# Kernel optimization log

Hardware: AMD Instinct MI355X
Metric: run time of the kernel (lower is better)

Reference implementation:

```python
import jax, jax.numpy as jnp
import numpy as np

EPS = 1e-5


def _knn_group(q, p, kk):
    """q: [3,Nq] query points, p: [3,M] reference points. Returns
    features [4,Nq,kk] = (residual xyz, distance) and neighbors [3,Nq,kk]."""
    qt, pt = q.T, p.T  # [Nq,3], [M,3]
    d2 = (jnp.sum(qt * qt, axis=1)[:, None]
          + jnp.sum(pt * pt, axis=1)[None, :]
          - 2.0 * qt @ pt.T)                       # [Nq,M] squared dists
    _, idx = jax.lax.top_k(-d2, kk)                 # kk nearest -> [Nq,kk]
    nn = pt[idx]                                    # [Nq,kk,3]
    resi = nn - qt[:, None, :]
    dist = jnp.linalg.norm(resi, axis=-1, keepdims=True)
    feat = jnp.concatenate([resi, dist], axis=-1)   # [Nq,kk,4]
    return feat.transpose(2, 0, 1), nn.transpose(2, 0, 1)


def _group_norm(x, groups, w, b):
    B, C, N, K = x.shape
    xg = x.reshape(B, groups, C // groups, N, K)
    mu = xg.mean(axis=(2, 3, 4), keepdims=True)
    var = xg.var(axis=(2, 3, 4), keepdims=True)
    xg = (xg - mu) * jax.lax.rsqrt(var + EPS)
    return xg.reshape(B, C, N, K) * w[None, :, None, None] + b[None, :, None, None]


def _forward(points0, points1, w1, b1, gn1_w, gn1_b, w2, b2, gn2_w, gn2_b,
             k, wt_np, perm_np):
    B, _, N = points0.shape
    feats, grouped = [], []
    for i in range(B):  # per-sample loop: split sizes are data-dependent (as in original)
        N0 = int(N * wt_np[i, 0]); N1 = N - N0
        k0 = int(k * wt_np[i, 0]); k1 = k - k0
        newp = jnp.concatenate([points0[i][:, perm_np[i, 0, :N0]],
                                points1[i][:, perm_np[i, 1, :N1]]], axis=-1)  # [3,N]
        f0, g0 = _knn_group(newp, points0[i], k0)
        f1, g1 = _knn_group(newp, points1[i], k1)
        feats.append(jnp.concatenate([f0, f1], axis=-1))
        grouped.append(jnp.concatenate([g0, g1], axis=-1))
    x = jnp.stack(feats)        # [B,4,N,k]
    gp = jnp.stack(grouped)     # [B,3,N,k]
    # 1x1 conv -> GroupNorm -> ReLU, twice
    x = jnp.einsum('bcnk,oc->bonk', x, w1) + b1[None, :, None, None]
    x = jax.nn.relu(_group_norm(x, w1.shape[0] // 8, gn1_w, gn1_b))
    x = jnp.einsum('bcnk,oc->bonk', x, w2) + b2[None, :, None, None]
    x = jax.nn.relu(_group_norm(x, w2.shape[0] // 8, gn2_w, gn2_b))
    scores = jnp.max(x, axis=1)                 # [B,N,k]
    wts = jax.nn.softmax(scores, axis=-1)       # softmax over neighbors
    return jnp.sum(wts[:, None, :, :] * gp, axis=-1)  # [B,3,N]


def setup_inputs() -> dict:
    key = jax.random.key(0)
    B, N, K = 8, 4096, 32
    C1, C2 = 32, 64
    ks = jax.random.split(key, 8)
    points0 = jax.random.normal(ks[0], (B, 3, N), jnp.float32)
    points1 = jax.random.normal(ks[1], (B, 3, N), jnp.float32)
    weighted_t = jax.random.uniform(ks[2], (B, 2), jnp.float32, 0.25, 0.75)
    perm = jax.vmap(lambda kk: jax.random.permutation(kk, N))(
        jax.random.split(ks[3], B * 2)).reshape(B, 2, N).astype(jnp.int32)
    w1 = 0.1 * jax.random.normal(ks[4], (C1, 4), jnp.float32)
    b1 = jnp.zeros((C1,), jnp.float32)
    gn1_w = jnp.ones((C1,), jnp.float32)
    gn1_b = jnp.zeros((C1,), jnp.float32)
    w2 = 0.1 * jax.random.normal(ks[5], (C2, C1), jnp.float32)
    b2 = jnp.zeros((C2,), jnp.float32)
    gn2_w = jnp.ones((C2,), jnp.float32)
    gn2_b = jnp.zeros((C2,), jnp.float32)
    return dict(points0=points0, points1=points1, k=K, weighted_t=weighted_t,
                perm=perm, w1=w1, b1=b1, gn1_w=gn1_w, gn1_b=gn1_b,
                w2=w2, b2=b2, gn2_w=gn2_w, gn2_b=gn2_b)


def reference(points0, points1, k, weighted_t, perm, w1, b1, gn1_w, gn1_b,
              w2, b2, gn2_w, gn2_b):
    wt_np = np.asarray(weighted_t)   # concrete: drives static split sizes
    perm_np = np.asarray(perm)
    return _forward(points0, points1, w1, b1, gn1_w, gn1_b, w2, b2,
                    gn2_w, gn2_b, int(k), wt_np, perm_np)
```

## Files before the change

### kernel.cpp

```cpp
#include <hip/hip_runtime.h>
#include <math.h>

#define RQ 6
constexpr int WRANKS = 768;
constexpr int WCH = 12;

typedef __attribute__((ext_vector_type(8))) short s8v;
typedef __attribute__((ext_vector_type(4))) float f32x4;

__device__ inline unsigned short f2bf(float x) {
    const unsigned int u = __float_as_uint(x);
    return (unsigned short)((u + 0x7FFFu + ((u >> 16) & 1u)) >> 16);
}

__constant__ float ZB[63] = {
    -2.1539f, -1.8627f, -1.6759f, -1.5341f, -1.4178f, -1.3180f, -1.2299f, -1.1503f,
    -1.0775f, -1.0100f, -0.9468f, -0.8871f, -0.8305f, -0.7764f, -0.7245f, -0.6745f,
    -0.6261f, -0.5791f, -0.5334f, -0.4888f, -0.4451f, -0.4023f, -0.3601f, -0.3186f,
    -0.2776f, -0.2372f, -0.1971f, -0.1573f, -0.1178f, -0.0784f, -0.0392f,  0.0000f,
     0.0392f,  0.0784f,  0.1178f,  0.1573f,  0.1971f,  0.2372f,  0.2776f,  0.3186f,
     0.3601f,  0.4023f,  0.4451f,  0.4888f,  0.5334f,  0.5791f,  0.6261f,  0.6745f,
     0.7245f,  0.7764f,  0.8305f,  0.8871f,  0.9468f,  1.0100f,  1.0775f,  1.1503f,
     1.2299f,  1.3180f,  1.4178f,  1.5341f,  1.6759f,  1.8627f,  2.1539f };

__global__ __launch_bounds__(1024) void zbin_kernel(
    const float* __restrict__ p0, const float* __restrict__ p1,
    float4* __restrict__ sp, int* __restrict__ starts, int N)
{
    __shared__ int cnt[64], off[64], cur[64];
    const int t = threadIdx.x;
    const int bl = blockIdx.x;
    const int b = bl >> 1, list = bl & 1;
    const float* rb = (list ? p1 : p0) + (size_t)(b * 3) * N;
    if (t < 64) { cnt[t] = 0; cur[t] = 0; }
    __syncthreads();
    int mybin[4]; float mx[4], my[4], mz[4];
    for (int i = 0; i < 4; ++i) {
        const int idx = i * 1024 + t;
        const float z = rb[2 * N + idx];
        mx[i] = rb[idx]; my[i] = rb[N + idx]; mz[i] = z;
        int bin = 0;
#pragma unroll
        for (int s = 32; s; s >>= 1)
            if (bin + s <= 63 && z >= ZB[bin + s - 1]) bin += s;
        mybin[i] = bin;
        atomicAdd(&cnt[bin], 1);
    }
    __syncthreads();
    if (t < 64) {
        const int v = cnt[t];
        int x = v;
#pragma unroll
        for (int o = 1; o < 64; o <<= 1) {
            const int y = __shfl_up(x, o);
            if (t >= o) x += y;
        }
        off[t] = x - v;
        starts[bl * 65 + t] = x - v;
        if (t == 63) starts[bl * 65 + 64] = x;
    }
    __syncthreads();
    for (int i = 0; i < 4; ++i) {
        const int bin = mybin[i];
        const int pos = off[bin] + atomicAdd(&cur[bin], 1);
        sp[(size_t)bl * 4096 + pos] =
            make_float4(mx[i], my[i], mz[i],
                        fmaf(mx[i], mx[i], fmaf(my[i], my[i], mz[i] * mz[i])));
    }
}


__device__ __forceinline__ void cpush(unsigned key, unsigned pos, unsigned Tu,
                                      bool valid,
                                      unsigned* __restrict__ ck,
                                      unsigned* __restrict__ cp,
                                      int& cnt)
{
    const bool pred = valid && (key <= Tu);
    const unsigned long long bal = __ballot(pred);
    const unsigned below = __builtin_amdgcn_mbcnt_hi(
        (unsigned)(bal >> 32), __builtin_amdgcn_mbcnt_lo((unsigned)bal, 0u));
    const unsigned idx = (unsigned)cnt + below;
    if (pred && idx < 64u) { ck[idx] = key; cp[idx] = pos; }
    cnt += (int)__popcll(bal);
}

__device__ __forceinline__ void cscan(const float4* __restrict__ L,
                                      int bs, int be,
                                      float qx, float qy, float qz, float qq,
                                      unsigned Tu,
                                      unsigned* __restrict__ ck,
                                      unsigned* __restrict__ cp,
                                      int& cnt, int lane)
{
    for (int p = bs; p < be; p += 64) {
        const int pos = p + lane;
        const float4 pc = L[min(pos, be - 1)];
        const float dt = fmaf(qz, pc.z, fmaf(qy, pc.y, qx * pc.x));
        const float d = fmaxf(fmaf(-2.f, dt, pc.w + qq), 0.f);
        cpush(__float_as_uint(d), (unsigned)pos, Tu, pos < be, ck, cp, cnt);
    }
}

__device__ __forceinline__ void sort2_write(
    const unsigned* __restrict__ ck0, const unsigned* __restrict__ cp0, int cnt0,
    const float4* __restrict__ L0, int kk0, int ob0,
    const unsigned* __restrict__ ck1, const unsigned* __restrict__ cp1, int cnt1,
    const float4* __restrict__ L1, int kk1, int ob1,
    float qx, float qy, float qz, float4* __restrict__ feat, int lane)
{
    unsigned vk0 = (lane < cnt0) ? ck0[lane] : 0xFFFFFFFFu;
    unsigned vp0 = (lane < cnt0) ? cp0[lane] : 0xFFFFFFFFu;
    unsigned vk1 = (lane < cnt1) ? ck1[lane] : 0xFFFFFFFFu;
    unsigned vp1 = (lane < cnt1) ? cp1[lane] : 0xFFFFFFFFu;
#pragma unroll
    for (int k2 = 2; k2 <= 64; k2 <<= 1) {
#pragma unroll
        for (int jj = k2 >> 1; jj; jj >>= 1) {
            const unsigned yk0 = __shfl_xor(vk0, jj), yp0 = __shfl_xor(vp0, jj);
            const unsigned yk1 = __shfl_xor(vk1, jj), yp1 = __shfl_xor(vp1, jj);
            const bool keepmin = (((lane & jj) == 0) == ((lane & k2) == 0));
            const bool lt0 = (vk0 < yk0) || ((vk0 == yk0) && (vp0 < yp0));
            const bool s0 = keepmin ? (!lt0) : lt0;
            vk0 = s0 ? yk0 : vk0; vp0 = s0 ? yp0 : vp0;
            const bool lt1 = (vk1 < yk1) || ((vk1 == yk1) && (vp1 < yp1));
            const bool s1 = keepmin ? (!lt1) : lt1;
            vk1 = s1 ? yk1 : vk1; vp1 = s1 ? yp1 : vp1;
        }
    }
    if (lane < kk0) {
        const float4 pc = L0[vp0 & 4095u];
        const float rx = pc.x - qx, ry = pc.y - qy, rz = pc.z - qz;
        feat[ob0 + lane] =
            make_float4(rx, ry, rz, sqrtf(fmaf(rx, rx, fmaf(ry, ry, rz * rz))));
    }
    if (lane < kk1) {
        const float4 pc = L1[vp1 & 4095u];
        const float rx = pc.x - qx, ry = pc.y - qy, rz = pc.z - qz;
        feat[ob1 + lane] =
            make_float4(rx, ry, rz, sqrtf(fmaf(rx, rx, fmaf(ry, ry, rz * rz))));
    }
}

__device__ __forceinline__ void sort_write(
    const unsigned* __restrict__ ck, const unsigned* __restrict__ cp, int cnt,
    const float4* __restrict__ L, int kk, int obase,
    float qx, float qy, float qz, float4* __restrict__ feat, int lane)
{
    unsigned vk = (lane < cnt) ? ck[lane] : 0xFFFFFFFFu;
    unsigned vp = (lane < cnt) ? cp[lane] : 0xFFFFFFFFu;
#pragma unroll
    for (int k2 = 2; k2 <= 64; k2 <<= 1) {
#pragma unroll
        for (int jj = k2 >> 1; jj; jj >>= 1) {
            const unsigned yk = __shfl_xor(vk, jj);
            const unsigned yp = __shfl_xor(vp, jj);
            const bool keepmin = (((lane & jj) == 0) == ((lane & k2) == 0));
            const bool lt = (vk < yk) || ((vk == yk) && (vp < yp));
            const bool sely = keepmin ? (!lt) : lt;
            vk = sely ? yk : vk;
            vp = sely ? yp : vp;
        }
    }
    if (lane < kk) {
        const float4 pc = L[vp & 4095u];
        const float rx = pc.x - qx, ry = pc.y - qy, rz = pc.z - qz;
        feat[obase + lane] =
            make_float4(rx, ry, rz, sqrtf(fmaf(rx, rx, fmaf(ry, ry, rz * rz))));
    }
}

__device__ __forceinline__ void qpush(unsigned (&kh)[RQ], unsigned (&kl)[RQ],
                                      unsigned key, unsigned pos)
{
    bool cb[RQ];
#pragma unroll
    for (int s = 0; s < RQ; ++s) cb[s] = key < kh[s];
#pragma unroll
    for (int s = RQ - 1; s >= 1; --s) {
        kh[s] = cb[s - 1] ? kh[s - 1] : (cb[s] ? key : kh[s]);
        kl[s] = cb[s - 1] ? kl[s - 1] : (cb[s] ? pos : kl[s]);
    }
    kh[0] = cb[0] ? key : kh[0];
    kl[0] = cb[0] ? pos : kl[0];
}

__device__ __forceinline__ void pop_extract(
    unsigned (&kh)[RQ], unsigned (&kl)[RQ], int kk,
    const float4* __restrict__ L, int obase,
    float qx, float qy, float qz, float4* __restrict__ feat, int lane)
{
    unsigned mwin = 0;
    for (int rr = 0; rr < kk; ++rr) {
        unsigned gg = kh[0];
#pragma unroll
        for (int off = 32; off; off >>= 1) gg = min(gg, __shfl_xor(gg, off));
        const bool tied = (kh[0] == gg);
        unsigned mc;
        const unsigned long long bal = __ballot(tied);
        if (bal & (bal - 1)) {
            mc = tied ? kl[0] : 0xFFFFFFFFu;
#pragma unroll
            for (int off = 32; off; off >>= 1) mc = min(mc, __shfl_xor(mc, off));
        } else {
            mc = __shfl(kl[0], (int)__ffsll((long long)bal) - 1);
        }
        const bool w = tied && (kl[0] == mc);
        if (lane == rr) mwin = mc;
#pragma unroll
        for (int s = 0; s < RQ - 1; ++s) {
            kh[s] = w ? kh[s + 1] : kh[s];
            kl[s] = w ? kl[s + 1] : kl[s];
        }
        kh[RQ - 1] = w ? 0xFFFFFFFFu : kh[RQ - 1];
        kl[RQ - 1] = w ? 0xFFFFFFFFu : kl[RQ - 1];
    }
    if (lane < kk) {
        const float4 pc = L[mwin & 4095u];
        const float rx = pc.x - qx, ry = pc.y - qy, rz = pc.z - qz;
        feat[obase + lane] =
            make_float4(rx, ry, rz, sqrtf(fmaf(rx, rx, fmaf(ry, ry, rz * rz))));
    }
}

__device__ __forceinline__ void fallback_full(
    const float4* __restrict__ L, int Npts, int kk, int obase,
    float qx, float qy, float qz, float qq,
    float4* __restrict__ feat, int lane)
{
    unsigned kh[RQ], kl[RQ];
#pragma unroll
    for (int s = 0; s < RQ; ++s) { kh[s] = 0xFFFFFFFFu; kl[s] = 0xFFFFFFFFu; }
    for (int p = 0; p < Npts; p += 64) {
        const int pos = p + lane;
        const float4 pc = L[min(pos, Npts - 1)];
        const float dt = fmaf(qz, pc.z, fmaf(qy, pc.y, qx * pc.x));
        const float d = fmaxf(fmaf(-2.f, dt, pc.w + qq), 0.f);
        const unsigned key = (pos < Npts) ? __float_as_uint(d) : 0xFFFFFFFFu;
        qpush(kh, kl, key, (unsigned)pos);
    }
    pop_extract(kh, kl, kk, L, obase, qx, qy, qz, feat, lane);
}

__global__ __launch_bounds__(256, 4) void knn_kernel(
    const float* __restrict__ p0, const float* __restrict__ p1,
    const float* __restrict__ wt, const int* __restrict__ perm,
    const float4* __restrict__ sp, const int* __restrict__ starts,
    float4* __restrict__ feat, float4* __restrict__ newp, int N)
{
    __shared__ unsigned ck0s[256], cp0s[256], ck1s[256], cp1s[256];
    const int lane = threadIdx.x & 63;
    const int wv = threadIdx.x >> 6;
    const int gwave = (int)((blockIdx.x * 256 + threadIdx.x) >> 6);
    const int b = gwave / N;
    const int n = gwave - b * N;
    const int q = b * N + n;

    unsigned* __restrict__ ck0 = ck0s + wv * 64;
    unsigned* __restrict__ cp0 = cp0s + wv * 64;
    unsigned* __restrict__ ck1 = ck1s + wv * 64;
    unsigned* __restrict__ cp1 = cp1s + wv * 64;

    const float wt0 = wt[b * 2];
    const int N0 = (int)(N * wt0);
    const int k0 = (int)(32 * wt0);
    const int kk0 = k0, kk1 = 32 - k0;

    int j; const float* src;
    if (n < N0) { j = perm[(b * 2) * N + n];            src = p0; }
    else        { j = perm[(b * 2 + 1) * N + (n - N0)]; src = p1; }
    const float qx = __uint_as_float(__builtin_amdgcn_readfirstlane(
                         __float_as_uint(src[(b * 3) * N + j])));
    const float qy = __uint_as_float(__builtin_amdgcn_readfirstlane(
                         __float_as_uint(src[(b * 3 + 1) * N + j])));
    const float qz = __uint_as_float(__builtin_amdgcn_readfirstlane(
                         __float_as_uint(src[(b * 3 + 2) * N + j])));
    const float qq = qx * qx + qy * qy + qz * qz;

    const int bl0 = b * 2, bl1 = b * 2 + 1;
    const int stv0 = starts[bl0 * 65 + lane];
    const int stv1 = starts[bl1 * 65 + lane];

    const float bv = (lane < 63) ? ZB[lane] : 3.0e38f;
    const int qbin = __popcll(__ballot(qz >= bv));

    if (lane == 0) newp[q] = make_float4(qx, qy, qz, 0.f);

    const float4* L0 = sp + (size_t)bl0 * 4096;
    const float4* L1 = sp + (size_t)bl1 * 4096;

    const int st0 = __shfl(stv0, qbin);
    const int en0 = (qbin >= 63) ? N : __shfl(stv0, qbin + 1);
    const int st1 = __shfl(stv1, qbin);
    const int en1 = (qbin >= 63) ? N : __shfl(stv1, qbin + 1);
    int s0 = ((st0 + en0) >> 1) - WRANKS / 2;
    s0 = s0 < 0 ? 0 : (s0 > N - WRANKS ? N - WRANKS : s0);
    int s1 = ((st1 + en1) >> 1) - WRANKS / 2;
    s1 = s1 < 0 ? 0 : (s1 > N - WRANKS ? N - WRANKS : s1);
    const int e0 = s0 + WRANKS, e1 = s1 + WRANKS;

    const float4* Lb0 = L0 + s0 + lane;
    const float4* Lb1 = L1 + s1 + lane;
    unsigned k0v[WCH], k1v[WCH];
    unsigned mn0 = 0xFFFFFFFFu, mn1 = 0xFFFFFFFFu;
    {
        float4 A0[3], A1[3], B0[3], B1[3];
#pragma unroll
        for (int c = 0; c < 3; ++c) { A0[c] = Lb0[c << 6]; A1[c] = Lb1[c << 6]; }
#pragma unroll
        for (int g = 0; g < 4; ++g) {
            if (g < 3) {
#pragma unroll
                for (int c = 0; c < 3; ++c) {
                    B0[c] = Lb0[(g * 3 + 3 + c) << 6];
                    B1[c] = Lb1[(g * 3 + 3 + c) << 6];
                }
            }
#pragma unroll
            for (int c = 0; c < 3; ++c) {
                const int ch = g * 3 + c;
                {
                    const float dt = fmaf(qz, A0[c].z, fmaf(qy, A0[c].y, qx * A0[c].x));
                    k0v[ch] = __float_as_uint(fmaxf(fmaf(-2.f, dt, A0[c].w + qq), 0.f));
                    mn0 = min(mn0, k0v[ch]);
                }
                {
                    const float dt = fmaf(qz, A1[c].z, fmaf(qy, A1[c].y, qx * A1[c].x));
                    k1v[ch] = __float_as_uint(fmaxf(fmaf(-2.f, dt, A1[c].w + qq), 0.f));
                    mn1 = min(mn1, k1v[ch]);
                }
            }
            if (g < 3) {
#pragma unroll
                for (int c = 0; c < 3; ++c) { A0[c] = B0[c]; A1[c] = B1[c]; }
            }
        }
    }

    unsigned x0 = mn0, x1 = mn1;
#pragma unroll
    for (int k2 = 2; k2 <= 64; k2 <<= 1) {
#pragma unroll
        for (int jj = k2 >> 1; jj; jj >>= 1) {
            const unsigned y0 = __shfl_xor(x0, jj);
            const unsigned y1 = __shfl_xor(x1, jj);
            const bool keepmin = (((lane & jj) == 0) == ((lane & k2) == 0));
            x0 = keepmin ? min(x0, y0) : (x0 > y0 ? x0 : y0);
            x1 = keepmin ? min(x1, y1) : (x1 > y1 ? x1 : y1);
        }
    }
    const unsigned Tu0 = (unsigned)__shfl((int)x0, kk0 - 1);
    const unsigned Tu1 = (unsigned)__shfl((int)x1, kk1 - 1);
    const float T0f = __uint_as_float(Tu0);
    const float T1f = __uint_as_float(Tu1);

    int cnt0 = 0, cnt1 = 0;
#pragma unroll
    for (int ch = 0; ch < WCH; ++ch) {
        cpush(k0v[ch], (unsigned)(s0 + (ch << 6) + lane), Tu0, true, ck0, cp0, cnt0);
        cpush(k1v[ch], (unsigned)(s1 + (ch << 6) + lane), Tu1, true, ck1, cp1, cnt1);
    }

    {
        const int binL = __popcll(__ballot(stv0 <= s0)) - 1;
        if (s0 > 0) {
            const int bs = __shfl(stv0, binL);
            if (bs < s0) cscan(L0, bs, s0, qx, qy, qz, qq, Tu0, ck0, cp0, cnt0, lane);
            for (int jb = binL - 1; jb >= 0; --jb) {
                const float dz = qz - ZB[jb];
                if (dz * dz * 0.99999f > T0f) break;
                const int bs2 = __shfl(stv0, jb);
                const int be2 = __shfl(stv0, jb + 1);
                cscan(L0, bs2, be2, qx, qy, qz, qq, Tu0, ck0, cp0, cnt0, lane);
            }
        }
        if (e0 < N) {
            const int binR = __popcll(__ballot(stv0 <= e0)) - 1;
            const int re = (binR >= 63) ? N : __shfl(stv0, binR + 1);
            if (e0 < re) cscan(L0, e0, re, qx, qy, qz, qq, Tu0, ck0, cp0, cnt0, lane);
            for (int jb = binR + 1; jb <= 63; ++jb) {
                const float dz = ZB[jb - 1] - qz;
                if (dz * dz * 0.99999f > T0f) break;
                const int bs2 = __shfl(stv0, jb);
                const int be2 = (jb >= 63) ? N : __shfl(stv0, jb + 1);
                cscan(L0, bs2, be2, qx, qy, qz, qq, Tu0, ck0, cp0, cnt0, lane);
            }
        }
        const int binL1 = __popcll(__ballot(stv1 <= s1)) - 1;
        if (s1 > 0) {
            const int bs = __shfl(stv1, binL1);
            if (bs < s1) cscan(L1, bs, s1, qx, qy, qz, qq, Tu1, ck1, cp1, cnt1, lane);
            for (int jb = binL1 - 1; jb >= 0; --jb) {
                const float dz = qz - ZB[jb];
                if (dz * dz * 0.99999f > T1f) break;
                const int bs2 = __shfl(stv1, jb);
                const int be2 = __shfl(stv1, jb + 1);
                cscan(L1, bs2, be2, qx, qy, qz, qq, Tu1, ck1, cp1, cnt1, lane);
            }
        }
        if (e1 < N) {
            const int binR1 = __popcll(__ballot(stv1 <= e1)) - 1;
            const int re = (binR1 >= 63) ? N : __shfl(stv1, binR1 + 1);
            if (e1 < re) cscan(L1, e1, re, qx, qy, qz, qq, Tu1, ck1, cp1, cnt1, lane);
            for (int jb = binR1 + 1; jb <= 63; ++jb) {
                const float dz = ZB[jb - 1] - qz;
                if (dz * dz * 0.99999f > T1f) break;
                const int bs2 = __shfl(stv1, jb);
                const int be2 = (jb >= 63) ? N : __shfl(stv1, jb + 1);
                cscan(L1, bs2, be2, qx, qy, qz, qq, Tu1, ck1, cp1, cnt1, lane);
            }
        }
    }

    const int ob0 = (q << 5), ob1 = (q << 5) + k0;
    if ((cnt0 <= 64) && (cnt1 <= 64)) {
        sort2_write(ck0, cp0, cnt0, L0, kk0, ob0,
                    ck1, cp1, cnt1, L1, kk1, ob1,
                    qx, qy, qz, feat, lane);
    } else {
        if (cnt0 <= 64) sort_write(ck0, cp0, cnt0, L0, kk0, ob0, qx, qy, qz, feat, lane);
        else            fallback_full(L0, N, kk0, ob0, qx, qy, qz, qq, feat, lane);
        if (cnt1 <= 64) sort_write(ck1, cp1, cnt1, L1, kk1, ob1, qx, qy, qz, feat, lane);
        else            fallback_full(L1, N, kk1, ob1, qx, qy, qz, qq, feat, lane);
    }
}

__global__ __launch_bounds__(256) void moment_stats_kernel(
    const float4* __restrict__ feat, float* __restrict__ stats1, int N)
{
    const int t = threadIdx.x, lane = t & 63;
    const int bpb = 64;
    const int b = blockIdx.x / bpb;
    const int ppb = (N * 32) / bpb;
    const size_t base = (size_t)b * N * 32 + (size_t)(blockIdx.x % bpb) * ppb;
    float a[14];
#pragma unroll
    for (int i = 0; i < 14; ++i) a[i] = 0.f;
    for (int i = t; i < ppb; i += 256) {
        const float4 f = feat[base + i];
        a[0] += f.x; a[1] += f.y; a[2] += f.z; a[3] += f.w;
        a[4] = fmaf(f.x, f.x, a[4]);  a[5] = fmaf(f.x, f.y, a[5]);
        a[6] = fmaf(f.x, f.z, a[6]);  a[7] = fmaf(f.x, f.w, a[7]);
        a[8] = fmaf(f.y, f.y, a[8]);  a[9] = fmaf(f.y, f.z, a[9]);
        a[10] = fmaf(f.y, f.w, a[10]); a[11] = fmaf(f.z, f.z, a[11]);
        a[12] = fmaf(f.z, f.w, a[12]); a[13] = fmaf(f.w, f.w, a[13]);
    }
#pragma unroll
    for (int i = 0; i < 14; ++i) {
        float x = a[i];
#pragma unroll
        for (int o = 32; o; o >>= 1) x += __shfl_down(x, o);
        a[i] = x;
    }
    __shared__ float sm[14];
    if (t < 14) sm[t] = 0.f;
    __syncthreads();
    if (lane == 0) {
#pragma unroll
        for (int i = 0; i < 14; ++i) atomicAdd(&sm[i], a[i]);
    }
    __syncthreads();
    if (t < 14) atomicAdd(&stats1[b * 14 + t], sm[t]);
}

template <int MODE>
__global__ __launch_bounds__(256) void conv2_pass_kernel(
    const float4* __restrict__ feat,
    const float* __restrict__ w1, const float* __restrict__ b1,
    const float* __restrict__ gn1w, const float* __restrict__ gn1b,
    const float* __restrict__ stats1,
    const float* __restrict__ w2, const float* __restrict__ b2,
    const float* __restrict__ gn2w, const float* __restrict__ gn2b,
    float* __restrict__ stats2,
    const float4* __restrict__ newp, float* __restrict__ out,
    int N, float inv_cnt)
{
    const int t = threadIdx.x, lane = t & 63, wv = t >> 6;
    const int quad = lane >> 4, col = lane & 15;
    const int bpb = (N * 32) / 512;
    const int b = blockIdx.x / bpb;
    const int pblock = (blockIdx.x - b * bpb) * 512;
    const size_t pbase = (size_t)b * N * 32 + pblock + wv * 128;

    __shared__ float sfin[24];
    __shared__ float sacc[16];
    __shared__ unsigned short h_lds[512 * 40];
    __shared__ float ssc[512];

    if (t < 16) sacc[t] = 0.f;
    if (t < 4) {
        const float cnt = (float)(N * 32);
        const float* mm = stats1 + b * 14;
        const float S0 = mm[0], S1 = mm[1], S2 = mm[2], S3 = mm[3];
        float sum = 0.f, sq = 0.f;
        for (int cch = 0; cch < 8; ++cch) {
            const int cid = t * 8 + cch;
            const float4 w = ((const float4*)w1)[cid];
            const float bb = b1[cid];
            const float ws = w.x * S0 + w.y * S1 + w.z * S2 + w.w * S3;
            const float wMw =
                w.x * w.x * mm[4] + w.y * w.y * mm[8] + w.z * w.z * mm[11] +
                w.w * w.w * mm[13] +
                2.f * (w.x * w.y * mm[5] + w.x * w.z * mm[6] + w.x * w.w * mm[7] +
                       w.y * w.z * mm[9] + w.y * w.w * mm[10] + w.z * w.w * mm[12]);
            sum += cnt * bb + ws;
            sq += cnt * bb * bb + 2.f * bb * ws + wMw;
        }
        const float mu = sum * inv_cnt, var = sq * inv_cnt - mu * mu;
        sfin[2 * t] = mu; sfin[2 * t + 1] = rsqrtf(var + 1e-5f);
    }
    if (MODE == 1 && t >= 4 && t < 12) {
        const int g = t - 4;
        const float S = stats2[b * 16 + g], Q = stats2[b * 16 + 8 + g];
        const float mu = S * inv_cnt, var = Q * inv_cnt - mu * mu;
        sfin[8 + 2 * g] = mu; sfin[8 + 2 * g + 1] = rsqrtf(var + 1e-5f);
    }
    __syncthreads();

    const int c1 = lane & 31, pt = lane >> 5;
    const float4 w1r = ((const float4*)w1)[c1];
    const float b1c = b1[c1];
    const int g1 = c1 >> 3;
    const float sc1 = sfin[2 * g1 + 1] * gn1w[c1];
    const float sh1 = gn1b[c1] - sfin[2 * g1] * sc1;

    for (int it = 0; it < 64; ++it) {
        const size_t p = pbase + it * 2;
        const float4 f = feat[p + pt];
        const float y = b1c + w1r.x * f.x + w1r.y * f.y + w1r.z * f.z + w1r.w * f.w;
        const float h = fmaxf(0.f, fmaf(y, sc1, sh1));
        h_lds[(wv * 128 + it * 2 + pt) * 40 + c1] = f2bf(h);
    }

    s8v afr[4];
#pragma unroll
    for (int T = 0; T < 4; ++T) {
        const int row = T * 16 + col;
#pragma unroll
        for (int j2 = 0; j2 < 8; ++j2)
            afr[T][j2] = (short)f2bf(w2[row * 32 + quad * 8 + j2]);
    }

    float b2v[4][4], sc2v[4][4], sh2v[4][4];
#pragma unroll
    for (int T = 0; T < 4; ++T)
#pragma unroll
        for (int r4 = 0; r4 < 4; ++r4) {
            const int cch = T * 16 + quad * 4 + r4;
            b2v[T][r4] = b2[cch];
            if (MODE == 1) {
                const int g2 = cch >> 3;
                const float sc = sfin[8 + 2 * g2 + 1] * gn2w[cch];
                sc2v[T][r4] = sc;
                sh2v[T][r4] = gn2b[cch] - sfin[8 + 2 * g2] * sc + b2[cch] * sc;
            }
        }

    float gsum[4] = {0, 0, 0, 0}, gsq[4] = {0, 0, 0, 0};

    for (int pt16 = 0; pt16 < 8; ++pt16) {
        const int row = wv * 128 + pt16 * 16 + col;
        const s8v bfr = *(const s8v*)&h_lds[row * 40 + quad * 8];
        f32x4 acc[4];
#pragma unroll
        for (int T = 0; T < 4; ++T) {
            acc[T] = (f32x4){0.f, 0.f, 0.f, 0.f};
            acc[T] = __builtin_amdgcn_mfma_f32_16x16x32_bf16(afr[T], bfr, acc[T], 0, 0, 0);
        }
        if (MODE == 0) {
#pragma unroll
            for (int T = 0; T < 4; ++T)
#pragma unroll
                for (int r4 = 0; r4 < 4; ++r4) {
                    const float v = acc[T][r4] + b2v[T][r4];
                    gsum[T] += v;
                    gsq[T] = fmaf(v, v, gsq[T]);
                }
        } else {
            float s = -3.0e38f;
#pragma unroll
            for (int T = 0; T < 4; ++T)
#pragma unroll
                for (int r4 = 0; r4 < 4; ++r4)
                    s = fmaxf(s, fmaxf(0.f, fmaf(acc[T][r4], sc2v[T][r4], sh2v[T][r4])));
            s = fmaxf(s, __shfl_xor(s, 16));
            s = fmaxf(s, __shfl_xor(s, 32));
            if (quad == 0) ssc[wv * 128 + pt16 * 16 + col] = s;
        }
    }

    if (MODE == 0) {
#pragma unroll
        for (int T = 0; T < 4; ++T) {
#pragma unroll
            for (int o = 1; o < 16; o <<= 1) {
                gsum[T] += __shfl_xor(gsum[T], o);
                gsq[T] += __shfl_xor(gsq[T], o);
            }
            gsum[T] += __shfl_xor(gsum[T], 16);
            gsq[T] += __shfl_xor(gsq[T], 16);
        }
        if (lane == 0) {
#pragma unroll
            for (int T = 0; T < 4; ++T) {
                atomicAdd(&sacc[2 * T], gsum[T]);
                atomicAdd(&sacc[8 + 2 * T], gsq[T]);
            }
        }
        if (lane == 32) {
#pragma unroll
            for (int T = 0; T < 4; ++T) {
                atomicAdd(&sacc[2 * T + 1], gsum[T]);
                atomicAdd(&sacc[8 + 2 * T + 1], gsq[T]);
            }
        }
        __syncthreads();
        if (t < 16) atomicAdd(&stats2[b * 16 + t], sacc[t]);
    } else {
        __syncthreads();
        const int qi = t >> 4, sub = t & 15;
        const int qg = (b * N * 32 + pblock) / 32 + qi;
        const int n = qg - b * N;
        const float s0 = ssc[qi * 32 + sub], s1 = ssc[qi * 32 + 16 + sub];
        float mx = fmaxf(s0, s1);
#pragma unroll
        for (int o = 8; o; o >>= 1) mx = fmaxf(mx, __shfl_xor(mx, o));
        const float e0 = __expf(s0 - mx), e1 = __expf(s1 - mx);
        float ssum = e0 + e1;
#pragma unroll
        for (int o = 8; o; o >>= 1) ssum += __shfl_xor(ssum, o);
        const float4 qc = newp[qg];
        const float4 f0 = feat[(size_t)qg * 32 + sub];
        const float4 f1 = feat[(size_t)qg * 32 + 16 + sub];
        float ax = e0 * (qc.x + f0.x) + e1 * (qc.x + f1.x);
        float ay = e0 * (qc.y + f0.y) + e1 * (qc.y + f1.y);
        float az = e0 * (qc.z + f0.z) + e1 * (qc.z + f1.z);
#pragma unroll
        for (int o = 8; o; o >>= 1) {
            ax += __shfl_xor(ax, o);
            ay += __shfl_xor(ay, o);
            az += __shfl_xor(az, o);
        }
        if (sub == 0) {
            const float inv = 1.f / ssum;
            out[(b * 3 + 0) * N + n] = ax * inv;
            out[(b * 3 + 1) * N + n] = ay * inv;
            out[(b * 3 + 2) * N + n] = az * inv;
        }
    }
}

extern "C" void kernel_launch(void* const* d_in, const int* in_sizes, int n_in,
                              void* d_out, int out_size, void* d_ws, size_t ws_size,
                              hipStream_t stream)
{
    const float* p0   = (const float*)d_in[0];
    const float* p1   = (const float*)d_in[1];
    const float* wt   = (const float*)d_in[3];
    const int*   perm = (const int*)d_in[4];
    const float* w1   = (const float*)d_in[5];
    const float* b1   = (const float*)d_in[6];
    const float* gn1w = (const float*)d_in[7];
    const float* gn1b = (const float*)d_in[8];
    const float* w2   = (const float*)d_in[9];
    const float* b2   = (const float*)d_in[10];
    const float* gn2w = (const float*)d_in[11];
    const float* gn2b = (const float*)d_in[12];
    float* out = (float*)d_out;

    const int B = in_sizes[3] / 2;
    const int N = in_sizes[0] / (3 * B);

    char* ws = (char*)d_ws;
    float4* spts = (float4*)ws;
    size_t off = (size_t)B * 2 * 4096 * sizeof(float4);
    float4* feat = (float4*)(ws + off);       off += (size_t)B * N * 32 * sizeof(float4);
    float4* newp = (float4*)(ws + off);       off += (size_t)B * N * sizeof(float4);
    float* stats1 = (float*)(ws + off);       off += (size_t)B * 14 * sizeof(float);
    float* stats2 = (float*)(ws + off);       off += (size_t)B * 16 * sizeof(float);
    int* starts = (int*)(ws + off);

    hipMemsetAsync(stats1, 0, (size_t)B * 30 * sizeof(float), stream);

    const float inv_cnt = 1.f / (8.f * (float)N * 32.f);

    zbin_kernel<<<B * 2, 1024, 0, stream>>>(p0, p1, spts, starts, N);

    knn_kernel<<<(B * N) / 4, 256, 0, stream>>>(
        p0, p1, wt, perm, spts, starts, feat, newp, N);

    moment_stats_kernel<<<B * 64, 256, 0, stream>>>(feat, stats1, N);

    conv2_pass_kernel<0><<<(B * N * 32) / 512, 256, 0, stream>>>(
        feat, w1, b1, gn1w, gn1b, stats1, w2, b2, gn2w, gn2b, stats2,
        newp, out, N, inv_cnt);

    conv2_pass_kernel<1><<<(B * N * 32) / 512, 256, 0, stream>>>(
        feat, w1, b1, gn1w, gn1b, stats1, w2, b2, gn2w, gn2b, stats2,
        newp, out, N, inv_cnt);
}
```

Baseline: 343.0 us.

## Split query gather into its own kernel, shrink KNN window, pack candidate LDS

Moves the permuted query-point gather out of the KNN kernel into a separate gather_kernel that writes newp, so each KNN wave reads one float4 instead of doing a dependent perm lookup and three scattered loads. It also shrinks the initial candidate window from 768 to 512 ranks (12 to 8 chunks), replaces the software-pipelined window load with a straight batch of loads, and packs key/position candidates into uint2 in LDS. The smaller window reduces register pressure and first-pass work, but gives a looser threshold, which can lead to more neighbor-bin scans or fallbacks. It also adds one extra kernel launch.

```diff
diff --git a/kernel.cpp b/kernel.cpp
--- a/kernel.cpp
+++ b/kernel.cpp
@@ -2,8 +2,8 @@
 #include <math.h>
 
 #define RQ 6
-constexpr int WRANKS = 768;
-constexpr int WCH = 12;
+constexpr int WRANKS = 512;
+constexpr int WCH = 8;
 
 typedef __attribute__((ext_vector_type(8))) short s8v;
 typedef __attribute__((ext_vector_type(4))) float f32x4;
@@ -69,11 +69,25 @@
     }
 }
 
+__global__ __launch_bounds__(256) void gather_kernel(
+    const float* __restrict__ p0, const float* __restrict__ p1,
+    const float* __restrict__ wt, const int* __restrict__ perm,
+    float4* __restrict__ newp, int N)
+{
+    const int q = blockIdx.x * 256 + threadIdx.x;
+    const int b = q / N, n = q - b * N;
+    const float wt0 = wt[b * 2];
+    const int N0 = (int)(N * wt0);
+    int j; const float* src;
+    if (n < N0) { j = perm[(b * 2) * N + n];            src = p0; }
+    else        { j = perm[(b * 2 + 1) * N + (n - N0)]; src = p1; }
+    newp[q] = make_float4(src[(b * 3) * N + j], src[(b * 3 + 1) * N + j],
+                          src[(b * 3 + 2) * N + j], 0.f);
+}
+
 
 __device__ __forceinline__ void cpush(unsigned key, unsigned pos, unsigned Tu,
-                                      bool valid,
-                                      unsigned* __restrict__ ck,
-                                      unsigned* __restrict__ cp,
+                                      bool valid, uint2* __restrict__ cc,
                                       int& cnt)
 {
     const bool pred = valid && (key <= Tu);
@@ -81,16 +95,14 @@
     const unsigned below = __builtin_amdgcn_mbcnt_hi(
         (unsigned)(bal >> 32), __builtin_amdgcn_mbcnt_lo((unsigned)bal, 0u));
     const unsigned idx = (unsigned)cnt + below;
-    if (pred && idx < 64u) { ck[idx] = key; cp[idx] = pos; }
+    if (pred && idx < 64u) cc[idx] = make_uint2(key, pos);
     cnt += (int)__popcll(bal);
 }
 
 __device__ __forceinline__ void cscan(const float4* __restrict__ L,
                                       int bs, int be,
                                       float qx, float qy, float qz, float qq,
-                                      unsigned Tu,
-                                      unsigned* __restrict__ ck,
-                                      unsigned* __restrict__ cp,
+                                      unsigned Tu, uint2* __restrict__ cc,
                                       int& cnt, int lane)
 {
     for (int p = bs; p < be; p += 64) {
@@ -98,21 +110,23 @@
         const float4 pc = L[min(pos, be - 1)];
         const float dt = fmaf(qz, pc.z, fmaf(qy, pc.y, qx * pc.x));
         const float d = fmaxf(fmaf(-2.f, dt, pc.w + qq), 0.f);
-        cpush(__float_as_uint(d), (unsigned)pos, Tu, pos < be, ck, cp, cnt);
+        cpush(__float_as_uint(d), (unsigned)pos, Tu, pos < be, cc, cnt);
     }
 }
 
 __device__ __forceinline__ void sort2_write(
-    const unsigned* __restrict__ ck0, const unsigned* __restrict__ cp0, int cnt0,
+    const uint2* __restrict__ cc0, int cnt0,
     const float4* __restrict__ L0, int kk0, int ob0,
-    const unsigned* __restrict__ ck1, const unsigned* __restrict__ cp1, int cnt1,
+    const uint2* __restrict__ cc1, int cnt1,
     const float4* __restrict__ L1, int kk1, int ob1,
     float qx, float qy, float qz, float4* __restrict__ feat, int lane)
 {
-    unsigned vk0 = (lane < cnt0) ? ck0[lane] : 0xFFFFFFFFu;
-    unsigned vp0 = (lane < cnt0) ? cp0[lane] : 0xFFFFFFFFu;
-    unsigned vk1 = (lane < cnt1) ? ck1[lane] : 0xFFFFFFFFu;
-    unsigned vp1 = (lane < cnt1) ? cp1[lane] : 0xFFFFFFFFu;
+    const uint2 v0 = cc0[lane];
+    const uint2 v1 = cc1[lane];
+    unsigned vk0 = (lane < cnt0) ? v0.x : 0xFFFFFFFFu;
+    unsigned vp0 = (lane < cnt0) ? v0.y : 0xFFFFFFFFu;
+    unsigned vk1 = (lane < cnt1) ? v1.x : 0xFFFFFFFFu;
+    unsigned vp1 = (lane < cnt1) ? v1.y : 0xFFFFFFFFu;
 #pragma unroll
     for (int k2 = 2; k2 <= 64; k2 <<= 1) {
 #pragma unroll
@@ -143,12 +157,13 @@
 }
 
 __device__ __forceinline__ void sort_write(
-    const unsigned* __restrict__ ck, const unsigned* __restrict__ cp, int cnt,
+    const uint2* __restrict__ cc, int cnt,
     const float4* __restrict__ L, int kk, int obase,
     float qx, float qy, float qz, float4* __restrict__ feat, int lane)
 {
-    unsigned vk = (lane < cnt) ? ck[lane] : 0xFFFFFFFFu;
-    unsigned vp = (lane < cnt) ? cp[lane] : 0xFFFFFFFFu;
+    const uint2 v = cc[lane];
+    unsigned vk = (lane < cnt) ? v.x : 0xFFFFFFFFu;
+    unsigned vp = (lane < cnt) ? v.y : 0xFFFFFFFFu;
 #pragma unroll
     for (int k2 = 2; k2 <= 64; k2 <<= 1) {
 #pragma unroll
@@ -243,12 +258,11 @@
 }
 
 __global__ __launch_bounds__(256, 4) void knn_kernel(
-    const float* __restrict__ p0, const float* __restrict__ p1,
-    const float* __restrict__ wt, const int* __restrict__ perm,
+    const float* __restrict__ wt,
     const float4* __restrict__ sp, const int* __restrict__ starts,
-    float4* __restrict__ feat, float4* __restrict__ newp, int N)
-{
-    __shared__ unsigned ck0s[256], cp0s[256], ck1s[256], cp1s[256];
+    float4* __restrict__ feat, const float4* __restrict__ newp, int N)
+{
+    __shared__ uint2 cc0s[256], cc1s[256];
     const int lane = threadIdx.x & 63;
     const int wv = threadIdx.x >> 6;
     const int gwave = (int)((blockIdx.x * 256 + threadIdx.x) >> 6);
@@ -256,25 +270,18 @@
     const int n = gwave - b * N;
     const int q = b * N + n;
 
-    unsigned* __restrict__ ck0 = ck0s + wv * 64;
-    unsigned* __restrict__ cp0 = cp0s + wv * 64;
-    unsigned* __restrict__ ck1 = ck1s + wv * 64;
-    unsigned* __restrict__ cp1 = cp1s + wv * 64;
-
-    const float wt0 = wt[b * 2];
-    const int N0 = (int)(N * wt0);
+    uint2* __restrict__ cc0 = cc0s + wv * 64;
+    uint2* __restrict__ cc1 = cc1s + wv * 64;
+
+    const float wt0 = __uint_as_float(__builtin_amdgcn_readfirstlane(
+                          __float_as_uint(wt[b * 2])));
     const int k0 = (int)(32 * wt0);
     const int kk0 = k0, kk1 = 32 - k0;
 
-    int j; const float* src;
-    if (n < N0) { j = perm[(b * 2) * N + n];            src = p0; }
-    else        { j = perm[(b * 2 + 1) * N + (n - N0)]; src = p1; }
-    const float qx = __uint_as_float(__builtin_amdgcn_readfirstlane(
-                         __float_as_uint(src[(b * 3) * N + j])));
-    const float qy = __uint_as_float(__builtin_amdgcn_readfirstlane(
-                         __float_as_uint(src[(b * 3 + 1) * N + j])));
-    const float qz = __uint_as_float(__builtin_amdgcn_readfirstlane(
-                         __float_as_uint(src[(b * 3 + 2) * N + j])));
+    const float4 qp = newp[q];
+    const float qx = __uint_as_float(__builtin_amdgcn_readfirstlane(__float_as_uint(qp.x)));
+    const float qy = __uint_as_float(__builtin_amdgcn_readfirstlane(__float_as_uint(qp.y)));
+    const float qz = __uint_as_float(__builtin_amdgcn_readfirstlane(__float_as_uint(qp.z)));
     const float qq = qx * qx + qy * qy + qz * qz;
 
     const int bl0 = b * 2, bl1 = b * 2 + 1;
@@ -283,8 +290,6 @@
 
     const float bv = (lane < 63) ? ZB[lane] : 3.0e38f;
     const int qbin = __popcll(__ballot(qz >= bv));
-
-    if (lane == 0) newp[q] = make_float4(qx, qy, qz, 0.f);
 
     const float4* L0 = sp + (size_t)bl0 * 4096;
     const float4* L1 = sp + (size_t)bl1 * 4096;
@@ -301,40 +306,22 @@
 
     const float4* Lb0 = L0 + s0 + lane;
     const float4* Lb1 = L1 + s1 + lane;
+    float4 P0v[WCH], P1v[WCH];
+#pragma unroll
+    for (int c = 0; c < WCH; ++c) P0v[c] = Lb0[c << 6];
+#pragma unroll
+    for (int c = 0; c < WCH; ++c) P1v[c] = Lb1[c << 6];
+
     unsigned k0v[WCH], k1v[WCH];
     unsigned mn0 = 0xFFFFFFFFu, mn1 = 0xFFFFFFFFu;
-    {
-        float4 A0[3], A1[3], B0[3], B1[3];
-#pragma unroll
-        for (int c = 0; c < 3; ++c) { A0[c] = Lb0[c << 6]; A1[c] = Lb1[c << 6]; }
-#pragma unroll
-        for (int g = 0; g < 4; ++g) {
-            if (g < 3) {
-#pragma unroll
-                for (int c = 0; c < 3; ++c) {
-                    B0[c] = Lb0[(g * 3 + 3 + c) << 6];
-                    B1[c] = Lb1[(g * 3 + 3 + c) << 6];
-                }
-            }
-#pragma unroll
-            for (int c = 0; c < 3; ++c) {
-                const int ch = g * 3 + c;
-                {
-                    const float dt = fmaf(qz, A0[c].z, fmaf(qy, A0[c].y, qx * A0[c].x));
-                    k0v[ch] = __float_as_uint(fmaxf(fmaf(-2.f, dt, A0[c].w + qq), 0.f));
-                    mn0 = min(mn0, k0v[ch]);
-                }
-                {
-                    const float dt = fmaf(qz, A1[c].z, fmaf(qy, A1[c].y, qx * A1[c].x));
-                    k1v[ch] = __float_as_uint(fmaxf(fmaf(-2.f, dt, A1[c].w + qq), 0.f));
-                    mn1 = min(mn1, k1v[ch]);
-                }
-            }
-            if (g < 3) {
-#pragma unroll
-                for (int c = 0; c < 3; ++c) { A0[c] = B0[c]; A1[c] = B1[c]; }
-            }
-        }
+#pragma unroll
+    for (int c = 0; c < WCH; ++c) {
+        const float dt0 = fmaf(qz, P0v[c].z, fmaf(qy, P0v[c].y, qx * P0v[c].x));
+        k0v[c] = __float_as_uint(fmaxf(fmaf(-2.f, dt0, P0v[c].w + qq), 0.f));
+        mn0 = min(mn0, k0v[c]);
+        const float dt1 = fmaf(qz, P1v[c].z, fmaf(qy, P1v[c].y, qx * P1v[c].x));
+        k1v[c] = __float_as_uint(fmaxf(fmaf(-2.f, dt1, P1v[c].w + qq), 0.f));
+        mn1 = min(mn1, k1v[c]);
     }
 
     unsigned x0 = mn0, x1 = mn1;
@@ -357,70 +344,70 @@
     int cnt0 = 0, cnt1 = 0;
 #pragma unroll
     for (int ch = 0; ch < WCH; ++ch) {
-        cpush(k0v[ch], (unsigned)(s0 + (ch << 6) + lane), Tu0, true, ck0, cp0, cnt0);
-        cpush(k1v[ch], (unsigned)(s1 + (ch << 6) + lane), Tu1, true, ck1, cp1, cnt1);
+        cpush(k0v[ch], (unsigned)(s0 + (ch << 6) + lane), Tu0, true, cc0, cnt0);
+        cpush(k1v[ch], (unsigned)(s1 + (ch << 6) + lane), Tu1, true, cc1, cnt1);
     }
 
     {
         const int binL = __popcll(__ballot(stv0 <= s0)) - 1;
         if (s0 > 0) {
             const int bs = __shfl(stv0, binL);
-            if (bs < s0) cscan(L0, bs, s0, qx, qy, qz, qq, Tu0, ck0, cp0, cnt0, lane);
+            if (bs < s0) cscan(L0, bs, s0, qx, qy, qz, qq, Tu0, cc0, cnt0, lane);
             for (int jb = binL - 1; jb >= 0; --jb) {
                 const float dz = qz - ZB[jb];
                 if (dz * dz * 0.99999f > T0f) break;
                 const int bs2 = __shfl(stv0, jb);
                 const int be2 = __shfl(stv0, jb + 1);
-                cscan(L0, bs2, be2, qx, qy, qz, qq, Tu0, ck0, cp0, cnt0, lane);
+                cscan(L0, bs2, be2, qx, qy, qz, qq, Tu0, cc0, cnt0, lane);
             }
         }
         if (e0 < N) {
             const int binR = __popcll(__ballot(stv0 <= e0)) - 1;
             const int re = (binR >= 63) ? N : __shfl(stv0, binR + 1);
-            if (e0 < re) cscan(L0, e0, re, qx, qy, qz, qq, Tu0, ck0, cp0, cnt0, lane);
+            if (e0 < re) cscan(L0, e0, re, qx, qy, qz, qq, Tu0, cc0, cnt0, lane);
             for (int jb = binR + 1; jb <= 63; ++jb) {
                 const float dz = ZB[jb - 1] - qz;
                 if (dz * dz * 0.99999f > T0f) break;
                 const int bs2 = __shfl(stv0, jb);
                 const int be2 = (jb >= 63) ? N : __shfl(stv0, jb + 1);
-                cscan(L0, bs2, be2, qx, qy, qz, qq, Tu0, ck0, cp0, cnt0, lane);
+                cscan(L0, bs2, be2, qx, qy, qz, qq, Tu0, cc0, cnt0, lane);
             }
         }
         const int binL1 = __popcll(__ballot(stv1 <= s1)) - 1;
         if (s1 > 0) {
             const int bs = __shfl(stv1, binL1);
-            if (bs < s1) cscan(L1, bs, s1, qx, qy, qz, qq, Tu1, ck1, cp1, cnt1, lane);
+            if (bs < s1) cscan(L1, bs, s1, qx, qy, qz, qq, Tu1, cc1, cnt1, lane);
             for (int jb = binL1 - 1; jb >= 0; --jb) {
                 const float dz = qz - ZB[jb];
                 if (dz * dz * 0.99999f > T1f) break;
                 const int bs2 = __shfl(stv1, jb);
                 const int be2 = __shfl(stv1, jb + 1);
-                cscan(L1, bs2, be2, qx, qy, qz, qq, Tu1, ck1, cp1, cnt1, lane);
+                cscan(L1, bs2, be2, qx, qy, qz, qq, Tu1, cc1, cnt1, lane);
             }
         }
         if (e1 < N) {
             const int binR1 = __popcll(__ballot(stv1 <= e1)) - 1;
             const int re = (binR1 >= 63) ? N : __shfl(stv1, binR1 + 1);
-            if (e1 < re) cscan(L1, e1, re, qx, qy, qz, qq, Tu1, ck1, cp1, cnt1, lane);
+            if (e1 < re) cscan(L1, e1, re, qx, qy, qz, qq, Tu1, cc1, cnt1, lane);
             for (int jb = binR1 + 1; jb <= 63; ++jb) {
                 const float dz = ZB[jb - 1] - qz;
                 if (dz * dz * 0.99999f > T1f) break;
                 const int bs2 = __shfl(stv1, jb);
                 const int be2 = (jb >= 63) ? N : __shfl(stv1, jb + 1);
-                cscan(L1, bs2, be2, qx, qy, qz, qq, Tu1, ck1, cp1, cnt1, lane);
+                cscan(L1, bs2, be2, qx, qy, qz, qq, Tu1, cc1, cnt1, lane);
             }
         }
     }
 
     const int ob0 = (q << 5), ob1 = (q << 5) + k0;
     if ((cnt0 <= 64) && (cnt1 <= 64)) {
-        sort2_write(ck0, cp0, cnt0, L0, kk0, ob0,
-                    ck1, cp1, cnt1, L1, kk1, ob1,
+        sort2_write(cc0, cnt0, L0, kk0, ob0,
+                    cc1, cnt1, L1, kk1, ob1,
                     qx, qy, qz, feat, lane);
     } else {
-        if (cnt0 <= 64) sort_write(ck0, cp0, cnt0, L0, kk0, ob0, qx, qy, qz, feat, lane);
+        if (cnt0 <= 64) sort_write(cc0, cnt0, L0, kk0, ob0, qx, qy, qz, feat, lane);
         else            fallback_full(L0, N, kk0, ob0, qx, qy, qz, qq, feat, lane);
-        if (cnt1 <= 64) sort_write(ck1, cp1, cnt1, L1, kk1, ob1, qx, qy, qz, feat, lane);
+        if (cnt1 <= 64) sort_write(cc1, cnt1, L1, kk1, ob1, qx, qy, qz, feat, lane);
         else            fallback_full(L1, N, kk1, ob1, qx, qy, qz, qq, feat, lane);
     }
 }
@@ -684,10 +671,12 @@
 
     const float inv_cnt = 1.f / (8.f * (float)N * 32.f);
 
+    gather_kernel<<<(B * N) / 256, 256, 0, stream>>>(p0, p1, wt, perm, newp, N);
+
     zbin_kernel<<<B * 2, 1024, 0, stream>>>(p0, p1, spts, starts, N);
 
     knn_kernel<<<(B * N) / 4, 256, 0, stream>>>(
-        p0, p1, wt, perm, spts, starts, feat, newp, N);
+        wt, spts, starts, feat, newp, N);
 
     moment_stats_kernel<<<B * 64, 256, 0, stream>>>(feat, stats1, N);
 
```

Measured after the change: 403.2 us. +17.6%, slower.
